# Performance work log

Hardware: AMD Instinct MI355X
Metric: run time of the kernel (lower is better)

The kernel has to match this reference:

```python
import jax, jax.numpy as jnp
import numpy as np

H = 4096          # hidden_size
NH = 32           # num_attention_heads
NKV = 2           # multi_query_group_num (kv heads)
HD = 128          # kv_channels / head_dim
RD = 64           # rotary_dim = head_dim * rotary_percent(0.5)
T = 2048          # total tokens (single prefill sequence)
EPS = 1e-5        # layernorm_epsilon
ROPE_BASE = 10000.0


def setup_inputs() -> dict:
    key = jax.random.key(0)
    k0, k1, k2, k3 = jax.random.split(key, 4)
    qkv_out = (NH + 2 * NKV) * HD  # 4608
    return {
        "positions": jnp.arange(T, dtype=jnp.int32),
        "hidden_states": jax.random.normal(k0, (T, H), jnp.float32),
        "w_qkv": jax.random.normal(k1, (qkv_out, H), jnp.float32) * 0.02,
        "b_qkv": jax.random.normal(k2, (qkv_out,), jnp.float32) * 0.02,
        "w_dense": jax.random.normal(k3, (H, NH * HD), jnp.float32) * 0.02,
        "q_ln_w": jnp.ones((HD,), jnp.float32),
        "k_ln_w": jnp.ones((HD,), jnp.float32),
    }


def _rmsnorm(x, w):
    # per-head RMSNorm over head_dim
    return x * jax.lax.rsqrt(jnp.mean(x * x, axis=-1, keepdims=True) + EPS) * w


def _rope(x, positions):
    # partial rotary (first RD dims), interleaved GPT-J style (is_neox_style=False)
    inv_freq = 1.0 / (ROPE_BASE ** (jnp.arange(0, RD, 2, dtype=jnp.float32) / RD))
    ang = positions.astype(jnp.float32)[:, None] * inv_freq      # [T, RD//2]
    cos = jnp.cos(ang)[:, None, :]                               # [T, 1, RD//2]
    sin = jnp.sin(ang)[:, None, :]
    x_rot, x_pass = x[..., :RD], x[..., RD:]
    x1 = x_rot[..., 0::2]
    x2 = x_rot[..., 1::2]
    r1 = x1 * cos - x2 * sin
    r2 = x2 * cos + x1 * sin
    x_rot = jnp.stack([r1, r2], axis=-1).reshape(x.shape[:-1] + (RD,))
    return jnp.concatenate([x_rot, x_pass], axis=-1)


def reference(positions, hidden_states, w_qkv, b_qkv, w_dense, q_ln_w, k_ln_w):
    qkv = hidden_states @ w_qkv.T + b_qkv                        # [T, 4608]
    q_size, kv_size = NH * HD, NKV * HD
    q = qkv[:, :q_size].reshape(T, NH, HD)
    k = qkv[:, q_size:q_size + kv_size].reshape(T, NKV, HD)
    v = qkv[:, q_size + kv_size:].reshape(T, NKV, HD)
    # optional qk layernorm (RMSNorm since config.rmsnorm)
    q = _rmsnorm(q, q_ln_w)
    k = _rmsnorm(k, k_ln_w)
    # rotary embedding
    q = _rope(q, positions)
    k = _rope(k, positions)
    # GQA: expand kv heads to query heads
    group = NH // NKV
    k_exp = jnp.repeat(k, group, axis=1)                         # [T, NH, HD]
    v_exp = jnp.repeat(v, group, axis=1)
    scale = HD ** -0.5
    scores = jnp.einsum("thd,shd->hts", q, k_exp) * scale        # [NH, T, T]
    causal = jnp.tril(jnp.ones((T, T), dtype=bool))
    scores = jnp.where(causal[None, :, :], scores, jnp.finfo(scores.dtype).min)
    attn = jax.nn.softmax(scores, axis=-1)
    out = jnp.einsum("hts,shd->thd", attn, v_exp).reshape(T, NH * HD)
    return out @ w_dense.T                                       # [T, H]
```

## Files before the change

### kernel.cpp

```cpp
#include <hip/hip_runtime.h>
#include <cstdint>
#include <cstddef>

typedef short short4v __attribute__((ext_vector_type(4)));
typedef short short8v __attribute__((ext_vector_type(8)));
typedef float f32x4   __attribute__((ext_vector_type(4)));

#define T_LEN  2048
#define HDIM   4096
#define NHEADS 32
#define HEADD  128
#define QKVN   4608

static __device__ __forceinline__ short f2bf(float f) {
  __bf16 h = (__bf16)f;
  return __builtin_bit_cast(short, h);
}
static __device__ __forceinline__ float bf2f(short u) {
  return __builtin_bit_cast(float, ((unsigned int)(unsigned short)u) << 16);
}

static __device__ __forceinline__ void gload_lds16(const void* g, void* l) {
  __builtin_amdgcn_global_load_lds((const __attribute__((address_space(1))) void*)g,
                                   (__attribute__((address_space(3))) void*)l,
                                   16, 0, 0);
}

__global__ void cast_f32_to_bf16(const float* __restrict__ in, short* __restrict__ out, int n4) {
  int idx = blockIdx.x * blockDim.x + threadIdx.x;
  int stride = gridDim.x * blockDim.x;
  const float4* in4 = (const float4*)in;
  short4v* out4 = (short4v*)out;
  for (int i = idx; i < n4; i += stride) {
    float4 v = in4[i];
    short4v o;
    o[0] = f2bf(v.x); o[1] = f2bf(v.y); o[2] = f2bf(v.z); o[3] = f2bf(v.w);
    out4[i] = o;
  }
}

template <int OUT_BF16>
__global__ __launch_bounds__(256, 2) void gemm_bt(
    const short* __restrict__ A,
    const short* __restrict__ B,
    const float* __restrict__ bias,
    void* __restrict__ Cout,
    int M, int N, int K)
{
  __shared__ short sA[128 * 64];
  __shared__ short sB[128 * 64];
  const int tid  = threadIdx.x;
  const int lane = tid & 63;
  const int wv   = tid >> 6;
  const int wr   = wv >> 1;
  const int wc   = wv & 1;

  const int nwg  = gridDim.x * gridDim.y;
  int wgid = blockIdx.y * gridDim.x + blockIdx.x;
  wgid = (wgid & 7) * (nwg >> 3) + (wgid >> 3);
  const int bn0 = (wgid / gridDim.y) * 128;
  const int bm0 = (wgid % gridDim.y) * 128;

  const int fr  = lane & 15;
  const int fkb = (lane >> 4) << 4;
  const int swz = (fr & 7) << 4;

  const int c_row  = tid >> 3;
  const int c_colb = (tid & 7) << 4;
  const int c_scol = (c_colb ^ ((c_row & 7) << 4)) >> 1;

  auto STAGE = [&](int kt) {
#pragma unroll
    for (int i = 0; i < 4; i++) {
      const int row = i * 32 + c_row;
      gload_lds16(A + (size_t)(bm0 + row) * K + kt + c_scol,
                  (char*)sA + (size_t)(i * 256 + wv * 64) * 16);
      gload_lds16(B + (size_t)(bn0 + row) * K + kt + c_scol,
                  (char*)sB + (size_t)(i * 256 + wv * 64) * 16);
    }
  };

  f32x4 zero = {0.f, 0.f, 0.f, 0.f};
  f32x4 acc[4][4];
#pragma unroll
  for (int m = 0; m < 4; m++)
#pragma unroll
    for (int n = 0; n < 4; n++) acc[m][n] = zero;

  for (int kt = 0; kt < K; kt += 64) {
    STAGE(kt);
    __syncthreads();
    const char* aB = (const char*)sA;
    const char* bB = (const char*)sB;
#pragma unroll
    for (int ks = 0; ks < 2; ks++) {
      short8v af[4], bfr[4];
#pragma unroll
      for (int m = 0; m < 4; m++) {
        const int row = wr * 64 + m * 16 + fr;
        af[m] = *(const short8v*)(aB + row * 128 + ((ks * 64 + fkb) ^ swz));
      }
#pragma unroll
      for (int n = 0; n < 4; n++) {
        const int row = wc * 64 + n * 16 + fr;
        bfr[n] = *(const short8v*)(bB + row * 128 + ((ks * 64 + fkb) ^ swz));
      }
#pragma unroll
      for (int m = 0; m < 4; m++)
#pragma unroll
        for (int n = 0; n < 4; n++)
          acc[m][n] = __builtin_amdgcn_mfma_f32_16x16x32_bf16(af[m], bfr[n], acc[m][n], 0, 0, 0);
    }
    __syncthreads();
  }

  const int rg = (lane >> 4) * 4;
#pragma unroll
  for (int m = 0; m < 4; m++) {
#pragma unroll
    for (int n = 0; n < 4; n++) {
      const int gcol = bn0 + wc * 64 + n * 16 + fr;
      const float bv = bias ? bias[gcol] : 0.0f;
#pragma unroll
      for (int j = 0; j < 4; j++) {
        const int grow = bm0 + wr * 64 + m * 16 + rg + j;
        const float v = acc[m][n][j] + bv;
        if (OUT_BF16)
          ((short*)Cout)[(size_t)grow * N + gcol] = f2bf(v);
        else
          ((float*)Cout)[(size_t)grow * N + gcol] = v;
      }
    }
  }
}

__global__ __launch_bounds__(64) void qkv_post_kernel(
    const short* __restrict__ qkvb,
    const int*   __restrict__ positions,
    const float* __restrict__ q_ln,
    const float* __restrict__ k_ln,
    short* __restrict__ Qb,
    short* __restrict__ Kb,
    short* __restrict__ Vt)
{
  const int t = blockIdx.x;
  const int h = blockIdx.y;
  const int lane = threadIdx.x;
  const unsigned int pk =
      ((const unsigned int*)(qkvb + (size_t)t * QKVN + h * HEADD))[lane];
  float x = bf2f((short)(pk & 0xffffu));
  float y = bf2f((short)(pk >> 16));

  if (h >= 34) {
    const int hv = h - 34;
    short* dst = Vt + ((size_t)hv * HEADD + 2 * lane) * T_LEN + t;
    dst[0]     = f2bf(x);
    dst[T_LEN] = f2bf(y);
    return;
  }

  float ss = x * x + y * y;
#pragma unroll
  for (int d = 32; d > 0; d >>= 1) ss += __shfl_xor(ss, d);
  const float r = rsqrtf(ss * (1.0f / 128.0f) + 1e-5f);
  const float* lnw = (h < 32) ? q_ln : k_ln;
  x = x * r * lnw[2 * lane];
  y = y * r * lnw[2 * lane + 1];

  if (lane < 32) {
    const float pos = (float)positions[t];
    const float ang = pos * powf(10000.0f, -(float)lane * (1.0f / 32.0f));
    const float c = cosf(ang), s = sinf(ang);
    const float r1 = x * c - y * s;
    const float r2 = y * c + x * s;
    x = r1; y = r2;
  }

  short* dst = (h < 32) ? (Qb + ((size_t)h * T_LEN + t) * HEADD + 2 * lane)
                        : (Kb + ((size_t)(h - 32) * T_LEN + t) * HEADD + 2 * lane);
  dst[0] = f2bf(x);
  dst[1] = f2bf(y);
}

__global__ __launch_bounds__(256, 2) void attn_kernel(
    const short* __restrict__ Qb,
    const short* __restrict__ Kb,
    const short* __restrict__ Vt,
    short* __restrict__ attn_out)
{
  __shared__ short Ks[2][64 * 128];
  __shared__ short Vs[2][128 * 64];
  __shared__ short pbuf[4][32 * 64];
  const int blk  = gridDim.x - 1 - blockIdx.x;
  const int h    = blockIdx.y;
  const int hkv  = h >> 4;
  const int tid  = threadIdx.x;
  const int lane = tid & 63;
  const int wv   = tid >> 6;
  const int B0   = blk * 128;
  const int qrow0 = B0 + wv * 32;
  const int fr = lane & 15;
  const int fk = (lane >> 4) * 8;
  const int fkb = (lane >> 4) << 4;
  const int rg = (lane >> 4) * 4;
  const int swz = (fr & 7) << 4;

  const short* Kh = Kb + (size_t)hkv * T_LEN * HEADD;
  const short* Vh = Vt + (size_t)hkv * HEADD * T_LEN;

  short8v qf[2][4];
#pragma unroll
  for (int g = 0; g < 2; g++) {
    const short* Qrow = Qb + ((size_t)h * T_LEN + qrow0 + g * 16 + fr) * HEADD + fk;
#pragma unroll
    for (int d0 = 0; d0 < 4; d0++) qf[g][d0] = *(const short8v*)(Qrow + d0 * 32);
  }

  float mrow[2][4], lrow[2][4];
#pragma unroll
  for (int g = 0; g < 2; g++)
#pragma unroll
    for (int j = 0; j < 4; j++) { mrow[g][j] = -1e30f; lrow[g][j] = 0.f; }
  f32x4 zero = {0.f, 0.f, 0.f, 0.f};
  f32x4 o[2][8];
#pragma unroll
  for (int g = 0; g < 2; g++)
#pragma unroll
    for (int d = 0; d < 8; d++) o[g][d] = zero;

  char* pb = (char*)&pbuf[wv][0];
  const float scale = 0.08838834764831845f;
  const int nt = 2 * blk + 2;

  auto STAGE = [&](int b, int t) {
    const int s0 = t * 64;
#pragma unroll
    for (int i = 0; i < 4; i++) {
      const int c    = i * 256 + tid;
      const int row  = c >> 4;
      const int colb = (c & 15) << 4;
      const int scol = (colb ^ ((row & 7) << 4)) >> 1;
      gload_lds16(Kh + (size_t)(s0 + row) * HEADD + scol,
                  (char*)&Ks[b][0] + (size_t)(i * 256 + wv * 64) * 16);
    }
#pragma unroll
    for (int i = 0; i < 4; i++) {
      const int c    = i * 256 + tid;
      const int row  = c >> 3;
      const int colb = (c & 7) << 4;
      const int scol = (colb ^ ((row & 7) << 4)) >> 1;
      gload_lds16(Vh + (size_t)row * T_LEN + s0 + scol,
                  (char*)&Vs[b][0] + (size_t)(i * 256 + wv * 64) * 16);
    }
  };

  int cur = 0;
  STAGE(0, 0);
  __syncthreads();

  for (int t = 0; t < nt; ++t) {
    if (t + 1 < nt) STAGE(cur ^ 1, t + 1);
    const int s0 = t * 64;
    const char* KsB = (const char*)&Ks[cur][0];
    const char* VsB = (const char*)&Vs[cur][0];

    float scv[2][4][4];
#pragma unroll
    for (int sub = 0; sub < 4; sub++) {
      const char* Kbase = KsB + (sub * 16 + fr) * 256;
      f32x4 a0 = zero, a1 = zero;
#pragma unroll
      for (int d0 = 0; d0 < 4; d0++) {
        short8v kf = *(const short8v*)(Kbase + ((d0 * 64 + fkb) ^ swz));
        a0 = __builtin_amdgcn_mfma_f32_16x16x32_bf16(qf[0][d0], kf, a0, 0, 0, 0);
        a1 = __builtin_amdgcn_mfma_f32_16x16x32_bf16(qf[1][d0], kf, a1, 0, 0, 0);
      }
#pragma unroll
      for (int j = 0; j < 4; j++) {
        scv[0][sub][j] = a0[j] * scale;
        scv[1][sub][j] = a1[j] * scale;
      }
    }
    if (t >= nt - 2) {
#pragma unroll
      for (int g = 0; g < 2; g++)
#pragma unroll
        for (int sub = 0; sub < 4; sub++) {
          const int colp = s0 + sub * 16 + fr;
#pragma unroll
          for (int j = 0; j < 4; j++)
            if (colp > qrow0 + g * 16 + rg + j) scv[g][sub][j] = -1e30f;
        }
    }
    float pmax[2][4];
#pragma unroll
    for (int g = 0; g < 2; g++)
#pragma unroll
      for (int j = 0; j < 4; j++)
        pmax[g][j] = fmaxf(fmaxf(scv[g][0][j], scv[g][1][j]),
                           fmaxf(scv[g][2][j], scv[g][3][j]));
    float growth = -1e30f;
#pragma unroll
    for (int g = 0; g < 2; g++)
#pragma unroll
      for (int j = 0; j < 4; j++) growth = fmaxf(growth, pmax[g][j] - mrow[g][j]);
    if (!__all(growth <= 8.0f)) {
#pragma unroll
      for (int g = 0; g < 2; g++)
#pragma unroll
        for (int j = 0; j < 4; j++) {
          float mx = pmax[g][j];
#pragma unroll
          for (int d = 1; d < 16; d <<= 1) mx = fmaxf(mx, __shfl_xor(mx, d));
          const float mn = fmaxf(mrow[g][j], mx);
          const float c  = __expf(mrow[g][j] - mn);
          mrow[g][j] = mn;
          lrow[g][j] *= c;
#pragma unroll
          for (int df = 0; df < 8; df++) o[g][df][j] *= c;
        }
    }
#pragma unroll
    for (int g = 0; g < 2; g++)
#pragma unroll
      for (int j = 0; j < 4; j++) {
        const int prow = g * 16 + rg + j;
        char* prb = pb + prow * 128;
        const int rswz = ((rg + j) & 7) << 4;
        float ps = 0.f;
#pragma unroll
        for (int sub = 0; sub < 4; sub++) {
          const float p = __expf(scv[g][sub][j] - mrow[g][j]);
          ps += p;
          *(short*)(prb + ((((sub * 16 + fr) << 1)) ^ rswz)) = f2bf(p);
        }
        lrow[g][j] += ps;
      }
    asm volatile("" ::: "memory");
    short8v pf[2][2];
#pragma unroll
    for (int g = 0; g < 2; g++)
#pragma unroll
      for (int ks = 0; ks < 2; ks++)
        pf[g][ks] = *(const short8v*)(pb + (g * 16 + fr) * 128 + ((ks * 64 + fkb) ^ swz));
#pragma unroll
    for (int df = 0; df < 8; df++) {
      const char* Vbase = VsB + (df * 16 + fr) * 128;
      short8v vf0 = *(const short8v*)(Vbase + ((0 + fkb) ^ swz));
      short8v vf1 = *(const short8v*)(Vbase + ((64 + fkb) ^ swz));
      o[0][df] = __builtin_amdgcn_mfma_f32_16x16x32_bf16(pf[0][0], vf0, o[0][df], 0, 0, 0);
      o[0][df] = __builtin_amdgcn_mfma_f32_16x16x32_bf16(pf[0][1], vf1, o[0][df], 0, 0, 0);
      o[1][df] = __builtin_amdgcn_mfma_f32_16x16x32_bf16(pf[1][0], vf0, o[1][df], 0, 0, 0);
      o[1][df] = __builtin_amdgcn_mfma_f32_16x16x32_bf16(pf[1][1], vf1, o[1][df], 0, 0, 0);
    }
    __syncthreads();
    cur ^= 1;
  }

#pragma unroll
  for (int g = 0; g < 2; g++)
#pragma unroll
    for (int j = 0; j < 4; j++) {
#pragma unroll
      for (int d = 1; d < 16; d <<= 1) lrow[g][j] += __shfl_xor(lrow[g][j], d);
    }
#pragma unroll
  for (int g = 0; g < 2; g++)
#pragma unroll
    for (int df = 0; df < 8; df++)
#pragma unroll
      for (int j = 0; j < 4; j++) {
        const float v = o[g][df][j] / lrow[g][j];
        attn_out[(size_t)(qrow0 + g * 16 + rg + j) * HDIM + h * HEADD + df * 16 + fr] = f2bf(v);
      }
}

extern "C" void kernel_launch(void* const* d_in, const int* in_sizes, int n_in,
                              void* d_out, int out_size, void* d_ws, size_t ws_size,
                              hipStream_t stream) {
  (void)out_size; (void)ws_size;
  int ip = 0, ih = 1, iwq = 2, ib = 3, iwd = 4, il0 = 5, il1 = 6;
  if (n_in == 7) {
    int p = -1, hh = -1, wq = -1, b = -1, wd = -1, l0 = -1, l1 = -1, ok = 1;
    for (int i = 0; i < 7; i++) {
      switch (in_sizes[i]) {
        case 2048:     p  = i; break;
        case 8388608:  hh = i; break;
        case 18874368: wq = i; break;
        case 4608:     b  = i; break;
        case 16777216: wd = i; break;
        case 128:      if (l0 < 0) l0 = i; else l1 = i; break;
        default:       ok = 0; break;
      }
    }
    if (ok && p >= 0 && hh >= 0 && wq >= 0 && b >= 0 && wd >= 0 && l0 >= 0 && l1 >= 0) {
      ip = p; ih = hh; iwq = wq; ib = b; iwd = wd; il0 = l0; il1 = l1;
    }
  }

  const int*   positions = (const int*)d_in[ip];
  const float* hidden    = (const float*)d_in[ih];
  const float* w_qkv     = (const float*)d_in[iwq];
  const float* b_qkv     = (const float*)d_in[ib];
  const float* w_dense   = (const float*)d_in[iwd];
  const float* q_ln      = (const float*)d_in[il0];
  const float* k_ln      = (const float*)d_in[il1];

  char* ws = (char*)d_ws;
  short* Ahs   = (short*)(ws + 0);
  short* Qb    = (short*)(ws + 0);
  short* Wqkv  = (short*)(ws + (size_t)16777216);
  short* Kb    = (short*)(ws + (size_t)16777216);
  short* Vt    = (short*)(ws + (size_t)17825792);
  short* Wd    = (short*)(ws + (size_t)18874368);
  short* qkvb  = (short*)(ws + (size_t)54525952);
  short* attnb = (short*)(ws + (size_t)54525952);

  cast_f32_to_bf16<<<dim3(1024), dim3(256), 0, stream>>>(hidden, Ahs, (T_LEN * HDIM) / 4);
  cast_f32_to_bf16<<<dim3(2048), dim3(256), 0, stream>>>(w_qkv, Wqkv, (QKVN * HDIM) / 4);
  gemm_bt<1><<<dim3(QKVN / 128, T_LEN / 128), dim3(256), 0, stream>>>(
      Ahs, Wqkv, b_qkv, (void*)qkvb, T_LEN, QKVN, HDIM);
  qkv_post_kernel<<<dim3(T_LEN, 36), dim3(64), 0, stream>>>(
      qkvb, positions, q_ln, k_ln, Qb, Kb, Vt);
  cast_f32_to_bf16<<<dim3(2048), dim3(256), 0, stream>>>(w_dense, Wd, (HDIM * HDIM) / 4);
  attn_kernel<<<dim3(16, NHEADS), dim3(256), 0, stream>>>(Qb, Kb, Vt, attnb);
  gemm_bt<0><<<dim3(HDIM / 128, T_LEN / 128), dim3(256), 0, stream>>>(
      attnb, Wd, nullptr, d_out, T_LEN, HDIM, HDIM);
}
```

Measured before the change: 324.7 us.

## Widen attention KV tile to 128, merge input casts, batch qkv_post heads

The attention kernel now stages 128-key K/V tiles in a single LDS buffer instead of double-buffered 64-key tiles. This halves the loop iterations and causal-mask passes, but global loads no longer overlap with compute because each tile is staged and synchronised before use. The two f32-to-bf16 casts for hidden states and QKV weights are merged into one launch. qkv_post now processes four heads per 256-thread block, cutting the block count.

```diff
diff --git a/kernel.cpp b/kernel.cpp
--- a/kernel.cpp
+++ b/kernel.cpp
@@ -24,6 +24,21 @@
   __builtin_amdgcn_global_load_lds((const __attribute__((address_space(1))) void*)g,
                                    (__attribute__((address_space(3))) void*)l,
                                    16, 0, 0);
+}
+
+__global__ void cast_pair(const float* __restrict__ a, short* __restrict__ oa, int na4,
+                          const float* __restrict__ b, short* __restrict__ ob, int nb4) {
+  int idx = blockIdx.x * blockDim.x + threadIdx.x;
+  int stride = gridDim.x * blockDim.x;
+  const int ntot = na4 + nb4;
+  for (int i = idx; i < ntot; i += stride) {
+    const float4* src = (i < na4) ? ((const float4*)a + i) : ((const float4*)b + (i - na4));
+    short4v* dst      = (i < na4) ? ((short4v*)oa + i)     : ((short4v*)ob + (i - na4));
+    float4 v = *src;
+    short4v o;
+    o[0] = f2bf(v.x); o[1] = f2bf(v.y); o[2] = f2bf(v.z); o[3] = f2bf(v.w);
+    *dst = o;
+  }
 }
 
 __global__ void cast_f32_to_bf16(const float* __restrict__ in, short* __restrict__ out, int n4) {
@@ -134,7 +149,7 @@
   }
 }
 
-__global__ __launch_bounds__(64) void qkv_post_kernel(
+__global__ __launch_bounds__(256) void qkv_post_kernel(
     const short* __restrict__ qkvb,
     const int*   __restrict__ positions,
     const float* __restrict__ q_ln,
@@ -144,8 +159,8 @@
     short* __restrict__ Vt)
 {
   const int t = blockIdx.x;
-  const int h = blockIdx.y;
-  const int lane = threadIdx.x;
+  const int h = blockIdx.y * 4 + (threadIdx.x >> 6);
+  const int lane = threadIdx.x & 63;
   const unsigned int pk =
       ((const unsigned int*)(qkvb + (size_t)t * QKVN + h * HEADD))[lane];
   float x = bf2f((short)(pk & 0xffffu));
@@ -188,8 +203,8 @@
     const short* __restrict__ Vt,
     short* __restrict__ attn_out)
 {
-  __shared__ short Ks[2][64 * 128];
-  __shared__ short Vs[2][128 * 64];
+  __shared__ short Ks[128 * 128];
+  __shared__ short Vs[128 * 128];
   __shared__ short pbuf[4][32 * 64];
   const int blk  = gridDim.x - 1 - blockIdx.x;
   const int h    = blockIdx.y;
@@ -230,43 +245,40 @@
 
   char* pb = (char*)&pbuf[wv][0];
   const float scale = 0.08838834764831845f;
-  const int nt = 2 * blk + 2;
-
-  auto STAGE = [&](int b, int t) {
-    const int s0 = t * 64;
-#pragma unroll
-    for (int i = 0; i < 4; i++) {
+  const int nt = blk + 1;
+
+  auto STAGE = [&](int t) {
+    const int s0 = t * 128;
+#pragma unroll
+    for (int i = 0; i < 8; i++) {
       const int c    = i * 256 + tid;
       const int row  = c >> 4;
       const int colb = (c & 15) << 4;
       const int scol = (colb ^ ((row & 7) << 4)) >> 1;
       gload_lds16(Kh + (size_t)(s0 + row) * HEADD + scol,
-                  (char*)&Ks[b][0] + (size_t)(i * 256 + wv * 64) * 16);
-    }
-#pragma unroll
-    for (int i = 0; i < 4; i++) {
+                  (char*)Ks + (size_t)(i * 256 + wv * 64) * 16);
+    }
+#pragma unroll
+    for (int i = 0; i < 8; i++) {
       const int c    = i * 256 + tid;
-      const int row  = c >> 3;
-      const int colb = (c & 7) << 4;
+      const int row  = c >> 4;
+      const int colb = (c & 15) << 4;
       const int scol = (colb ^ ((row & 7) << 4)) >> 1;
       gload_lds16(Vh + (size_t)row * T_LEN + s0 + scol,
-                  (char*)&Vs[b][0] + (size_t)(i * 256 + wv * 64) * 16);
+                  (char*)Vs + (size_t)(i * 256 + wv * 64) * 16);
     }
   };
 
-  int cur = 0;
-  STAGE(0, 0);
-  __syncthreads();
-
   for (int t = 0; t < nt; ++t) {
-    if (t + 1 < nt) STAGE(cur ^ 1, t + 1);
-    const int s0 = t * 64;
-    const char* KsB = (const char*)&Ks[cur][0];
-    const char* VsB = (const char*)&Vs[cur][0];
-
-    float scv[2][4][4];
-#pragma unroll
-    for (int sub = 0; sub < 4; sub++) {
+    STAGE(t);
+    __syncthreads();
+    const int s0 = t * 128;
+    const char* KsB = (const char*)Ks;
+    const char* VsB = (const char*)Vs;
+
+    float scv[2][8][4];
+#pragma unroll
+    for (int sub = 0; sub < 8; sub++) {
       const char* Kbase = KsB + (sub * 16 + fr) * 256;
       f32x4 a0 = zero, a1 = zero;
 #pragma unroll
@@ -281,11 +293,11 @@
         scv[1][sub][j] = a1[j] * scale;
       }
     }
-    if (t >= nt - 2) {
+    if (t == nt - 1) {
 #pragma unroll
       for (int g = 0; g < 2; g++)
 #pragma unroll
-        for (int sub = 0; sub < 4; sub++) {
+        for (int sub = 0; sub < 8; sub++) {
           const int colp = s0 + sub * 16 + fr;
 #pragma unroll
           for (int j = 0; j < 4; j++)
@@ -296,9 +308,13 @@
 #pragma unroll
     for (int g = 0; g < 2; g++)
 #pragma unroll
-      for (int j = 0; j < 4; j++)
-        pmax[g][j] = fmaxf(fmaxf(scv[g][0][j], scv[g][1][j]),
-                           fmaxf(scv[g][2][j], scv[g][3][j]));
+      for (int j = 0; j < 4; j++) {
+        float m0 = fmaxf(fmaxf(scv[g][0][j], scv[g][1][j]),
+                         fmaxf(scv[g][2][j], scv[g][3][j]));
+        float m1 = fmaxf(fmaxf(scv[g][4][j], scv[g][5][j]),
+                         fmaxf(scv[g][6][j], scv[g][7][j]));
+        pmax[g][j] = fmaxf(m0, m1);
+      }
     float growth = -1e30f;
 #pragma unroll
     for (int g = 0; g < 2; g++)
@@ -321,40 +337,43 @@
         }
     }
 #pragma unroll
-    for (int g = 0; g < 2; g++)
-#pragma unroll
-      for (int j = 0; j < 4; j++) {
-        const int prow = g * 16 + rg + j;
-        char* prb = pb + prow * 128;
-        const int rswz = ((rg + j) & 7) << 4;
-        float ps = 0.f;
-#pragma unroll
-        for (int sub = 0; sub < 4; sub++) {
-          const float p = __expf(scv[g][sub][j] - mrow[g][j]);
-          ps += p;
-          *(short*)(prb + ((((sub * 16 + fr) << 1)) ^ rswz)) = f2bf(p);
+    for (int half = 0; half < 2; half++) {
+#pragma unroll
+      for (int g = 0; g < 2; g++)
+#pragma unroll
+        for (int j = 0; j < 4; j++) {
+          const int prow = g * 16 + rg + j;
+          char* prb = pb + prow * 128;
+          const int rswz = ((rg + j) & 7) << 4;
+          float ps = 0.f;
+#pragma unroll
+          for (int s4 = 0; s4 < 4; s4++) {
+            const float p = __expf(scv[g][half * 4 + s4][j] - mrow[g][j]);
+            ps += p;
+            *(short*)(prb + ((((s4 * 16 + fr) << 1)) ^ rswz)) = f2bf(p);
+          }
+          lrow[g][j] += ps;
         }
-        lrow[g][j] += ps;
-      }
-    asm volatile("" ::: "memory");
-    short8v pf[2][2];
-#pragma unroll
-    for (int g = 0; g < 2; g++)
-#pragma unroll
-      for (int ks = 0; ks < 2; ks++)
-        pf[g][ks] = *(const short8v*)(pb + (g * 16 + fr) * 128 + ((ks * 64 + fkb) ^ swz));
-#pragma unroll
-    for (int df = 0; df < 8; df++) {
-      const char* Vbase = VsB + (df * 16 + fr) * 128;
-      short8v vf0 = *(const short8v*)(Vbase + ((0 + fkb) ^ swz));
-      short8v vf1 = *(const short8v*)(Vbase + ((64 + fkb) ^ swz));
-      o[0][df] = __builtin_amdgcn_mfma_f32_16x16x32_bf16(pf[0][0], vf0, o[0][df], 0, 0, 0);
-      o[0][df] = __builtin_amdgcn_mfma_f32_16x16x32_bf16(pf[0][1], vf1, o[0][df], 0, 0, 0);
-      o[1][df] = __builtin_amdgcn_mfma_f32_16x16x32_bf16(pf[1][0], vf0, o[1][df], 0, 0, 0);
-      o[1][df] = __builtin_amdgcn_mfma_f32_16x16x32_bf16(pf[1][1], vf1, o[1][df], 0, 0, 0);
+      asm volatile("" ::: "memory");
+      short8v pf[2][2];
+#pragma unroll
+      for (int g = 0; g < 2; g++)
+#pragma unroll
+        for (int ks = 0; ks < 2; ks++)
+          pf[g][ks] = *(const short8v*)(pb + (g * 16 + fr) * 128 + ((ks * 64 + fkb) ^ swz));
+#pragma unroll
+      for (int df = 0; df < 8; df++) {
+        const char* Vbase = VsB + (df * 16 + fr) * 256;
+        short8v vf0 = *(const short8v*)(Vbase + ((half * 128 + 0 + fkb) ^ swz));
+        short8v vf1 = *(const short8v*)(Vbase + ((half * 128 + 64 + fkb) ^ swz));
+        o[0][df] = __builtin_amdgcn_mfma_f32_16x16x32_bf16(pf[0][0], vf0, o[0][df], 0, 0, 0);
+        o[0][df] = __builtin_amdgcn_mfma_f32_16x16x32_bf16(pf[0][1], vf1, o[0][df], 0, 0, 0);
+        o[1][df] = __builtin_amdgcn_mfma_f32_16x16x32_bf16(pf[1][0], vf0, o[1][df], 0, 0, 0);
+        o[1][df] = __builtin_amdgcn_mfma_f32_16x16x32_bf16(pf[1][1], vf1, o[1][df], 0, 0, 0);
+      }
+      asm volatile("" ::: "memory");
     }
     __syncthreads();
-    cur ^= 1;
   }
 
 #pragma unroll
@@ -416,11 +435,11 @@
   short* qkvb  = (short*)(ws + (size_t)54525952);
   short* attnb = (short*)(ws + (size_t)54525952);
 
-  cast_f32_to_bf16<<<dim3(1024), dim3(256), 0, stream>>>(hidden, Ahs, (T_LEN * HDIM) / 4);
-  cast_f32_to_bf16<<<dim3(2048), dim3(256), 0, stream>>>(w_qkv, Wqkv, (QKVN * HDIM) / 4);
+  cast_pair<<<dim3(3072), dim3(256), 0, stream>>>(
+      hidden, Ahs, (T_LEN * HDIM) / 4, w_qkv, Wqkv, (QKVN * HDIM) / 4);
   gemm_bt<1><<<dim3(QKVN / 128, T_LEN / 128), dim3(256), 0, stream>>>(
       Ahs, Wqkv, b_qkv, (void*)qkvb, T_LEN, QKVN, HDIM);
-  qkv_post_kernel<<<dim3(T_LEN, 36), dim3(64), 0, stream>>>(
+  qkv_post_kernel<<<dim3(T_LEN, 9), dim3(256), 0, stream>>>(
       qkvb, positions, q_ln, k_ln, Qb, Kb, Vt);
   cast_f32_to_bf16<<<dim3(2048), dim3(256), 0, stream>>>(w_dense, Wd, (HDIM * HDIM) / 4);
   attn_kernel<<<dim3(16, NHEADS), dim3(256), 0, stream>>>(Qb, Kb, Vt, attnb);
```

Measured after the change: 352.3 us. 8.5% more time.
